# Performance work log

Measured on AMD Instinct MI355X. Metric: run time of the kernel, lower is better.

Reference implementation:

```python
import jax, jax.numpy as jnp
import numpy as np

EMBED = 1024
HEADS = 16
HEAD_DIM = EMBED // HEADS
NUM_BUCKETS = 32
MAX_DISTANCE = 128
B, L = 4, 2048


def relative_position_bucket(relative_position, num_buckets=NUM_BUCKETS, max_distance=MAX_DISTANCE):
    # Faithful port of the torch helper (unidirectional T5 bucketing).
    n = -relative_position                       # [L, L] int32
    max_exact = num_buckets // 2
    is_small = n < max_exact
    nf = jnp.maximum(n, 1).astype(jnp.float32)   # guard log(<=0); masked out by is_small
    val_if_large = max_exact + (
        jnp.log(nf / max_exact) / np.log(max_distance / max_exact) * (num_buckets - max_exact)
    ).astype(jnp.int32)                          # .long() in torch truncates; values >=0 here
    val_if_large = jnp.minimum(val_if_large, num_buckets - 1)
    ret = jnp.where(is_small, n, val_if_large)
    return jnp.maximum(ret, 0)


def setup_inputs() -> dict:
    key = jax.random.key(0)
    ks = jax.random.split(key, 11)
    s = 0.02
    return {
        "x": jax.random.normal(ks[0], (B, L, EMBED), dtype=jnp.float32),
        "wq": jax.random.normal(ks[1], (EMBED, EMBED), dtype=jnp.float32) * s,
        "bq": jnp.zeros((EMBED,), dtype=jnp.float32),
        "wk": jax.random.normal(ks[2], (EMBED, EMBED), dtype=jnp.float32) * s,
        "bk": jnp.zeros((EMBED,), dtype=jnp.float32),
        "wv": jax.random.normal(ks[3], (EMBED, EMBED), dtype=jnp.float32) * s,
        "bv": jnp.zeros((EMBED,), dtype=jnp.float32),
        "wo": jax.random.normal(ks[4], (EMBED, EMBED), dtype=jnp.float32) * s,
        "bo": jnp.zeros((EMBED,), dtype=jnp.float32),
        "rel_bias": jax.random.normal(ks[5], (NUM_BUCKETS, HEADS), dtype=jnp.float32) * s,
    }


def reference(x, wq, bq, wk, bk, wv, bv, wo, bo, rel_bias):
    Bx, Lx, C = x.shape
    # torch nn.Linear: y = x @ W.T + b
    def proj(w, b):
        y = jnp.einsum("blc,dc->bld", x, w) + b
        return y.reshape(Bx, Lx, HEADS, HEAD_DIM).transpose(0, 2, 1, 3)  # [B,H,L,Dh]
    q = proj(wq, bq)
    k = proj(wk, bk)
    v = proj(wv, bv)
    scores = jnp.einsum("bhqd,bhkd->bhqk", q, k) / np.sqrt(HEAD_DIM)  # [B,H,L,L]
    ctx = jnp.arange(Lx, dtype=jnp.int32)
    relative = ctx[None, :] - ctx[:, None]                            # [L,L]
    bucket_ids = relative_position_bucket(relative)                   # [L,L]
    bias = rel_bias[bucket_ids]                                       # [L,L,H]
    bias = jnp.transpose(bias, (2, 0, 1))                             # [H,L,L]
    attn = jax.nn.softmax(scores + bias[None], axis=-1)
    out = jnp.einsum("bhqk,bhkd->bhqd", attn, v)                      # [B,H,L,Dh]
    out = out.transpose(0, 2, 1, 3).reshape(Bx, Lx, C)
    return jnp.einsum("blc,dc->bld", out, wo) + bo
```

## Files before the change

kernel.cpp:

```cpp
#include <hip/hip_runtime.h>

typedef __bf16 bf16x8 __attribute__((ext_vector_type(8)));
typedef __bf16 bf16x2 __attribute__((ext_vector_type(2)));
typedef float f32x4 __attribute__((ext_vector_type(4)));
typedef float f32x16 __attribute__((ext_vector_type(16)));
typedef short short8v __attribute__((ext_vector_type(8)));
typedef unsigned uint4v __attribute__((ext_vector_type(4)));
typedef unsigned short ushort_t;

#define EMB 1024
#define HEADS 16
#define HDIM 64
#define BATCH 4
#define SEQ 2048
#define LOG2E 1.44269504088896340736f
#define FIXED_M 12.0f

__device__ __forceinline__ ushort_t f2bf(float f) {
  union { float f; unsigned u; } x; x.f = f;
  unsigned r = x.u + 0x7fffu + ((x.u >> 16) & 1u);
  return (ushort_t)(r >> 16);
}

__device__ __forceinline__ unsigned pack2(float lo, float hi) {
  bf16x2 t;
  t.x = (__bf16)lo;
  t.y = (__bf16)hi;
  return __builtin_bit_cast(unsigned, t);
}

__device__ __forceinline__ void gload_lds16(const void* g, void* l) {
  __builtin_amdgcn_global_load_lds(
      (const __attribute__((address_space(1))) void*)g,
      (__attribute__((address_space(3))) void*)l, 16, 0, 0);
}

__global__ __launch_bounds__(256) void convert_all(
    const float* __restrict__ x,
    const float* __restrict__ wq, const float* __restrict__ wk,
    const float* __restrict__ wv, const float* __restrict__ wo,
    ushort_t* __restrict__ xb, ushort_t* __restrict__ wqb,
    ushort_t* __restrict__ wkb, ushort_t* __restrict__ wvb,
    ushort_t* __restrict__ wob) {
  int cid = blockIdx.x * 256 + threadIdx.x;
  const float* src;
  ushort_t* dst;
  int off;
  if (cid < 1048576) {
    src = x; dst = xb; off = cid;
  } else {
    int r = cid - 1048576;
    int wi = r >> 17;
    off = r & 131071;
    src = wi == 0 ? wq : wi == 1 ? wk : wi == 2 ? wv : wo;
    dst = wi == 0 ? wqb : wi == 1 ? wkb : wi == 2 ? wvb : wob;
  }
  const float4* s4 = (const float4*)(src + (size_t)off * 8);
  float4 a = s4[0], b = s4[1];
  ushort_t tmp[8] = {f2bf(a.x), f2bf(a.y), f2bf(a.z), f2bf(a.w),
                     f2bf(b.x), f2bf(b.y), f2bf(b.z), f2bf(b.w)};
  *(short8v*)(dst + (size_t)off * 8) = *(const short8v*)tmp;
}

__global__ __launch_bounds__(256) void build_biasR(
    const float* __restrict__ rel_bias, float* __restrict__ biasR) {
  int fid = blockIdx.x * 256 + threadIdx.x;
  int hh = fid >> 12;
  int p = (fid >> 10) & 3;
  int j = fid & 1023;
#pragma unroll
  for (int e = 0; e < 4; ++e) {
    int r = 4 * j + p + e;
    int n = 2048 - r;
    int bucket;
    if (n < 16) {
      bucket = n > 0 ? n : 0;
    } else {
      float tt = logf((float)n * 0.0625f) * (16.0f / logf(8.0f));
      int v = 16 + (int)tt;
      bucket = v < 31 ? v : 31;
    }
    biasR[(size_t)fid * 4 + e] = rel_bias[bucket * HEADS + hh] * LOG2E - FIXED_M;
  }
}

__global__ __launch_bounds__(256) void gemm_qkv(
    const ushort_t* __restrict__ xb,
    const ushort_t* __restrict__ wqb, const ushort_t* __restrict__ wkb,
    const ushort_t* __restrict__ wvb,
    const float* __restrict__ bq, const float* __restrict__ bk,
    const float* __restrict__ bv,
    ushort_t* __restrict__ qb, ushort_t* __restrict__ kb,
    ushort_t* __restrict__ vtb) {
  const int wgid = blockIdx.x;
  const int xcd = wgid & 7;
  const int r0 = wgid >> 3;
  const int nb = r0 % 24;
  const int mb = (r0 / 24) * 8 + xcd;
  const int wsel = nb >> 3;
  const int nloc = (nb & 7) * 128;
  const ushort_t* W = wsel == 0 ? wqb : wsel == 1 ? wkb : wvb;
  const float* bias = wsel == 0 ? bq : wsel == 1 ? bk : bv;
  const float scale = wsel == 0 ? 0.125f * LOG2E : 1.0f;

  __shared__ ushort_t Al[128 * 64];
  __shared__ ushort_t Bl[128 * 64];
  const int tid = threadIdx.x, lane = tid & 63, wid = tid >> 6;
  const int wm = wid >> 1, wn = wid & 1;
  const int srow = lane >> 3;
  const int scol = (lane & 7) * 8;
  f32x4 acc[4][4] = {};

  for (int kt = 0; kt < EMB / 64; ++kt) {
    const int k0 = kt * 64;
#pragma unroll
    for (int i = 0; i < 4; ++i) {
      int c = i * 4 + wid;
      int row = c * 8 + srow;
      gload_lds16(xb + (size_t)(mb * 128 + row) * EMB + k0 + scol, &Al[c * 512]);
      gload_lds16(W + (size_t)(nloc + row) * EMB + k0 + scol, &Bl[c * 512]);
    }
    __syncthreads();
#pragma unroll
    for (int kk = 0; kk < 2; ++kk) {
      const int koff = kk * 32 + (lane >> 4) * 8;
      bf16x8 af[4], bfv[4];
#pragma unroll
      for (int m = 0; m < 4; ++m)
        af[m] = *(const bf16x8*)&Al[(wm * 64 + m * 16 + (lane & 15)) * 64 + koff];
#pragma unroll
      for (int n = 0; n < 4; ++n)
        bfv[n] = *(const bf16x8*)&Bl[(wn * 64 + n * 16 + (lane & 15)) * 64 + koff];
#pragma unroll
      for (int m = 0; m < 4; ++m)
#pragma unroll
        for (int n = 0; n < 4; ++n)
          acc[m][n] = __builtin_amdgcn_mfma_f32_16x16x32_bf16(af[m], bfv[n],
                                                              acc[m][n], 0, 0, 0);
    }
    __syncthreads();
  }

#pragma unroll
  for (int m = 0; m < 4; ++m)
#pragma unroll
    for (int n = 0; n < 4; ++n)
#pragma unroll
      for (int r = 0; r < 4; ++r) {
        int row = mb * 128 + wm * 64 + m * 16 + (lane >> 4) * 4 + r;
        int col = nloc + wn * 64 + n * 16 + (lane & 15);
        float v = (acc[m][n][r] + bias[col]) * scale;
        int b = row >> 11, l = row & 2047;
        int hh = col >> 6, d = col & 63;
        if (wsel == 2) {
          int lp = (l & ~12) | ((l & 4) << 1) | ((l & 8) >> 1);
          vtb[(((size_t)(b * HEADS + hh) * HDIM) + d) * SEQ + lp] = f2bf(v);
        } else {
          ushort_t* outp = wsel == 0 ? qb : kb;
          outp[(((size_t)(b * HEADS + hh) * SEQ) + l) * HDIM + d] = f2bf(v);
        }
      }
}

__global__ __launch_bounds__(256) void gemm_out(
    const ushort_t* __restrict__ ctxb, const ushort_t* __restrict__ wob,
    const float* __restrict__ bo, float* __restrict__ out) {
  const int wgid = blockIdx.x;
  const int xcd = wgid & 7;
  const int r0 = wgid >> 3;
  const int nb = r0 & 7;
  const int mb = (r0 >> 3) * 8 + xcd;
  __shared__ ushort_t Al[128 * 64];
  __shared__ ushort_t Bl[128 * 64];
  const int tid = threadIdx.x, lane = tid & 63, wid = tid >> 6;
  const int wm = wid >> 1, wn = wid & 1;
  const int srow = lane >> 3;
  const int scol = (lane & 7) * 8;
  f32x4 acc[4][4] = {};

  for (int kt = 0; kt < EMB / 64; ++kt) {
    const int k0 = kt * 64;
#pragma unroll
    for (int i = 0; i < 4; ++i) {
      int c = i * 4 + wid;
      int row = c * 8 + srow;
      gload_lds16(ctxb + (size_t)(mb * 128 + row) * EMB + k0 + scol, &Al[c * 512]);
      gload_lds16(wob + (size_t)(nb * 128 + row) * EMB + k0 + scol, &Bl[c * 512]);
    }
    __syncthreads();
#pragma unroll
    for (int kk = 0; kk < 2; ++kk) {
      const int koff = kk * 32 + (lane >> 4) * 8;
      bf16x8 af[4], bfv[4];
#pragma unroll
      for (int m = 0; m < 4; ++m)
        af[m] = *(const bf16x8*)&Al[(wm * 64 + m * 16 + (lane & 15)) * 64 + koff];
#pragma unroll
      for (int n = 0; n < 4; ++n)
        bfv[n] = *(const bf16x8*)&Bl[(wn * 64 + n * 16 + (lane & 15)) * 64 + koff];
#pragma unroll
      for (int m = 0; m < 4; ++m)
#pragma unroll
        for (int n = 0; n < 4; ++n)
          acc[m][n] = __builtin_amdgcn_mfma_f32_16x16x32_bf16(af[m], bfv[n],
                                                              acc[m][n], 0, 0, 0);
    }
    __syncthreads();
  }

#pragma unroll
  for (int m = 0; m < 4; ++m)
#pragma unroll
    for (int n = 0; n < 4; ++n)
#pragma unroll
      for (int r = 0; r < 4; ++r) {
        int row = mb * 128 + wm * 64 + m * 16 + (lane >> 4) * 4 + r;
        int col = nb * 128 + wn * 64 + n * 16 + (lane & 15);
        out[(size_t)row * EMB + col] = acc[m][n][r] + bo[col];
      }
}

__global__ __launch_bounds__(256) void attn(
    const ushort_t* __restrict__ qb, const ushort_t* __restrict__ kb,
    const ushort_t* __restrict__ vtb, const float* __restrict__ biasR,
    ushort_t* __restrict__ ctxb) {
  const int wgid = blockIdx.x;
  const int xcd = wgid & 7;
  const int sidx = wgid >> 3;
  const int qblk = sidx & 15;
  const int bh = ((sidx >> 4) << 3) | xcd;
  const int h = bh & 15, b = bh >> 4;
  const int tid = threadIdx.x;
  const int lane = tid & 63, w = tid >> 6;
  const int l31 = lane & 31, hi5 = lane >> 5;
  const int pidx = (lane ^ 32) << 2;

  __shared__ ushort_t SM[16384];

  const size_t base = (size_t)bh * (SEQ * HDIM);
  const int q = qblk * 128 + w * 32 + l31;

  bf16x8 qf[4];
#pragma unroll
  for (int s = 0; s < 4; ++s)
    qf[s] = *(const bf16x8*)&qb[base + (size_t)q * HDIM + s * 16 + hi5 * 8];

  int koA[4];
#pragma unroll
  for (int s = 0; s < 4; ++s)
    koA[s] = (s * 16 + hi5 * 8) ^ ((l31 & 7) << 3);
  const int rb0 = l31 * 64;
  const int rb1 = rb0 + 2048;

  const int p = (4 - (q & 3)) & 3;
  const int j00 = ((4 * hi5 - q + 2048) - p) >> 2;
  const float4* bptr = (const float4*)biasR + ((h * 4 + p) * 1024 + j00);

  const int chR0 = tid >> 3, chC0 = (tid & 7) * 8;
  const int chR1 = chR0 + 32;
  const int kd0 = chR0 * 64 + (chC0 ^ ((chR0 & 7) << 3));
  const int kd1 = chR1 * 64 + (chC0 ^ ((chR1 & 7) << 3));

  const ushort_t* kp0 = kb + base + (size_t)chR0 * HDIM + chC0;
  const ushort_t* kp1 = kb + base + (size_t)chR1 * HDIM + chC0;
  const ushort_t* vp0 = vtb + base + (size_t)chR0 * SEQ + chC0;
  const ushort_t* vp1 = vtb + base + (size_t)chR1 * SEQ + chC0;

  short8v kr0 = *(const short8v*)kp0;
  short8v kr1 = *(const short8v*)kp1;
  short8v vr0 = *(const short8v*)vp0;
  short8v vr1 = *(const short8v*)vp1;
  *(short8v*)&SM[kd0] = kr0;
  *(short8v*)&SM[kd1] = kr1;
  *(short8v*)&SM[4096 + kd0] = vr0;
  *(short8v*)&SM[4096 + kd1] = vr1;
  kp0 += 64 * HDIM; kp1 += 64 * HDIM; vp0 += 64; vp1 += 64;
  kr0 = *(const short8v*)kp0;
  kr1 = *(const short8v*)kp1;
  vr0 = *(const short8v*)vp0;
  vr1 = *(const short8v*)vp1;
  __syncthreads();

  f32x16 o0 = {}, o1 = {}, lv = {};

#pragma unroll 2
  for (int t = 0; t < 32; ++t) {
    const int c = t & 1;
    ushort_t* Kl = SM + c * 8192;
    ushort_t* Vl = Kl + 4096;

    float4 bw[8];
#pragma unroll
    for (int hh = 0; hh < 2; ++hh)
#pragma unroll
      for (int g = 0; g < 4; ++g)
        bw[hh * 4 + g] = bptr[hh * 8 + g * 2];

    f32x16 s0, s1;
#pragma unroll
    for (int r = 0; r < 16; ++r) {
      s0[r] = bw[r >> 2][r & 3];
      s1[r] = bw[4 + (r >> 2)][r & 3];
    }
    __builtin_amdgcn_s_setprio(1);
#pragma unroll
    for (int s = 0; s < 4; ++s) {
      bf16x8 ka = *(const bf16x8*)&Kl[rb0 + koA[s]];
      s0 = __builtin_amdgcn_mfma_f32_32x32x16_bf16(ka, qf[s], s0, 0, 0, 0);
    }
#pragma unroll
    for (int s = 0; s < 4; ++s) {
      bf16x8 ka = *(const bf16x8*)&Kl[rb1 + koA[s]];
      s1 = __builtin_amdgcn_mfma_f32_32x32x16_bf16(ka, qf[s], s1, 0, 0, 0);
    }
    __builtin_amdgcn_s_setprio(0);

    if (t < 31) {
      ushort_t* Kn = SM + (c ^ 1) * 8192;
      *(short8v*)&Kn[kd0] = kr0;
      *(short8v*)&Kn[kd1] = kr1;
      *(short8v*)&Kn[4096 + kd0] = vr0;
      *(short8v*)&Kn[4096 + kd1] = vr1;
      kp0 += 64 * HDIM; kp1 += 64 * HDIM; vp0 += 64; vp1 += 64;
      kr0 = *(const short8v*)kp0;
      kr1 = *(const short8v*)kp1;
      vr0 = *(const short8v*)vp0;
      vr1 = *(const short8v*)vp1;
    }

#pragma unroll
    for (int r = 0; r < 16; ++r) s0[r] = __builtin_amdgcn_exp2f(s0[r]);
#pragma unroll
    for (int r = 0; r < 16; ++r) s1[r] = __builtin_amdgcn_exp2f(s1[r]);
    lv += s0;
    lv += s1;

    unsigned pk0[8], pk1[8];
#pragma unroll
    for (int d = 0; d < 8; ++d) {
      pk0[d] = pack2(s0[2 * d], s0[2 * d + 1]);
      pk1[d] = pack2(s1[2 * d], s1[2 * d + 1]);
    }
    bf16x8 paf[4];
    {
      uint4v t0 = {pk0[0], pk0[1], pk0[2], pk0[3]};
      uint4v t1 = {pk0[4], pk0[5], pk0[6], pk0[7]};
      uint4v t2 = {pk1[0], pk1[1], pk1[2], pk1[3]};
      uint4v t3 = {pk1[4], pk1[5], pk1[6], pk1[7]};
      paf[0] = __builtin_bit_cast(bf16x8, t0);
      paf[1] = __builtin_bit_cast(bf16x8, t1);
      paf[2] = __builtin_bit_cast(bf16x8, t2);
      paf[3] = __builtin_bit_cast(bf16x8, t3);
    }

    __builtin_amdgcn_s_setprio(1);
#pragma unroll
    for (int ss = 0; ss < 4; ++ss) {
      bf16x8 vb0 = *(const bf16x8*)&Vl[rb0 + koA[ss]];
      bf16x8 vb1 = *(const bf16x8*)&Vl[rb1 + koA[ss]];
      o0 = __builtin_amdgcn_mfma_f32_32x32x16_bf16(paf[ss], vb0, o0, 0, 0, 0);
      o1 = __builtin_amdgcn_mfma_f32_32x32x16_bf16(paf[ss], vb1, o1, 0, 0, 0);
    }
    __builtin_amdgcn_s_setprio(0);

    if (t < 31) __syncthreads();
    bptr += 16;
  }

  float li = (((lv[0] + lv[1]) + (lv[2] + lv[3])) +
              ((lv[4] + lv[5]) + (lv[6] + lv[7]))) +
             (((lv[8] + lv[9]) + (lv[10] + lv[11])) +
              ((lv[12] + lv[13]) + (lv[14] + lv[15])));
  float li2 = __int_as_float(
      __builtin_amdgcn_ds_bpermute(pidx, __float_as_int(li)));
  li += li2;
  float inv = 1.0f / li;
#pragma unroll
  for (int r = 0; r < 16; ++r) {
    int qr = (r & 3) + 8 * (r >> 2) + 4 * hi5;
    float iv = __int_as_float(
        __builtin_amdgcn_ds_bpermute(qr << 2, __float_as_int(inv)));
    o0[r] *= iv;
    o1[r] *= iv;
  }
  ushort_t* T = SM + w * 2048;
#pragma unroll
  for (int r = 0; r < 16; ++r) {
    int qr = (r & 3) + 8 * (r >> 2) + 4 * hi5;
    int sw = (qr & 7) << 3;
    T[qr * 64 + (l31 ^ sw)] = f2bf(o0[r]);
    T[qr * 64 + ((32 + l31) ^ sw)] = f2bf(o1[r]);
  }
  const int qr2 = lane >> 1;
  const int dh0 = (lane & 1) * 32;
  const int sw2 = (qr2 & 7) << 3;
  const size_t crow =
      ((size_t)b * SEQ + qblk * 128 + w * 32 + qr2) * EMB + h * 64;
#pragma unroll
  for (int c = 0; c < 4; ++c) {
    short8v vv = *(const short8v*)&T[qr2 * 64 + ((dh0 + c * 8) ^ sw2)];
    *(short8v*)&ctxb[crow + dh0 + c * 8] = vv;
  }
}

extern "C" void kernel_launch(void* const* d_in, const int* in_sizes, int n_in,
                              void* d_out, int out_size, void* d_ws, size_t ws_size,
                              hipStream_t stream) {
  const float* x = (const float*)d_in[0];
  const float* wq = (const float*)d_in[1];
  const float* bq = (const float*)d_in[2];
  const float* wk = (const float*)d_in[3];
  const float* bk = (const float*)d_in[4];
  const float* wv = (const float*)d_in[5];
  const float* bv = (const float*)d_in[6];
  const float* wo = (const float*)d_in[7];
  const float* bo = (const float*)d_in[8];
  const float* rel_bias = (const float*)d_in[9];
  float* out = (float*)d_out;

  char* ws = (char*)d_ws;
  ushort_t* xb  = (ushort_t*)(ws);
  ushort_t* wqb = (ushort_t*)(ws + 16777216);
  ushort_t* wkb = (ushort_t*)(ws + 16777216 + 2097152);
  ushort_t* wvb = (ushort_t*)(ws + 16777216 + 2 * 2097152);
  ushort_t* wob = (ushort_t*)(ws + 16777216 + 3 * 2097152);
  ushort_t* qb  = (ushort_t*)(ws + 25165824);
  ushort_t* kb  = (ushort_t*)(ws + 25165824 + 16777216);
  ushort_t* vtb = (ushort_t*)(ws + 25165824 + 2 * 16777216);
  float* biasR  = (float*)(ws + 75497472);
  ushort_t* ctxb = xb;

  convert_all<<<6144, 256, 0, stream>>>(x, wq, wk, wv, wo, xb, wqb, wkb, wvb, wob);
  build_biasR<<<256, 256, 0, stream>>>(rel_bias, biasR);
  gemm_qkv<<<1536, 256, 0, stream>>>(xb, wqb, wkb, wvb, bq, bk, bv, qb, kb, vtb);
  attn<<<1024, 256, 0, stream>>>(qb, kb, vtb, biasR, ctxb);
  gemm_out<<<512, 256, 0, stream>>>(ctxb, wob, bo, out);
}
```

Baseline: 272.5 us.

## Stream K/V tiles into LDS with direct global-to-LDS loads

Replaces the register-staged K/V prefetch (global load into VGPRs, then ds_write into the other buffer) with a gload_lds16 helper that copies global memory straight into the double-buffered LDS tiles. The swizzle moves from the LDS write address to the global column offset. This frees the staging registers and drops the explicit LDS store instructions. It also shrinks the row-sum accumulator from 16 to 4 floats to cut register pressure. Correctness now depends on the async LDS loads completing before the barrier and on the new swizzle matching the read pattern.

```diff
diff --git a/kernel.cpp b/kernel.cpp
--- a/kernel.cpp
+++ b/kernel.cpp
@@ -256,38 +256,30 @@
   const int j00 = ((4 * hi5 - q + 2048) - p) >> 2;
   const float4* bptr = (const float4*)biasR + ((h * 4 + p) * 1024 + j00);
 
-  const int chR0 = tid >> 3, chC0 = (tid & 7) * 8;
-  const int chR1 = chR0 + 32;
-  const int kd0 = chR0 * 64 + (chC0 ^ ((chR0 & 7) << 3));
-  const int kd1 = chR1 * 64 + (chC0 ^ ((chR1 & 7) << 3));
-
-  const ushort_t* kp0 = kb + base + (size_t)chR0 * HDIM + chC0;
-  const ushort_t* kp1 = kb + base + (size_t)chR1 * HDIM + chC0;
-  const ushort_t* vp0 = vtb + base + (size_t)chR0 * SEQ + chC0;
-  const ushort_t* vp1 = vtb + base + (size_t)chR1 * SEQ + chC0;
-
-  short8v kr0 = *(const short8v*)kp0;
-  short8v kr1 = *(const short8v*)kp1;
-  short8v vr0 = *(const short8v*)vp0;
-  short8v vr1 = *(const short8v*)vp1;
-  *(short8v*)&SM[kd0] = kr0;
-  *(short8v*)&SM[kd1] = kr1;
-  *(short8v*)&SM[4096 + kd0] = vr0;
-  *(short8v*)&SM[4096 + kd1] = vr1;
+  const int srowK = lane >> 3;
+  const int scol8 = ((lane & 7) ^ srowK) * 8;
+  const int row0 = w * 16 + srowK;
+  const ushort_t* kp0 = kb + base + (size_t)row0 * HDIM + scol8;
+  const ushort_t* kp1 = kp0 + 8 * HDIM;
+  const ushort_t* vp0 = vtb + base + (size_t)row0 * SEQ + scol8;
+  const ushort_t* vp1 = vp0 + 8 * SEQ;
+  const int kdst0 = (2 * w) * 512, kdst1 = kdst0 + 512;
+
+  gload_lds16(kp0, SM + kdst0);
+  gload_lds16(kp1, SM + kdst1);
+  gload_lds16(vp0, SM + 4096 + kdst0);
+  gload_lds16(vp1, SM + 4096 + kdst1);
   kp0 += 64 * HDIM; kp1 += 64 * HDIM; vp0 += 64; vp1 += 64;
-  kr0 = *(const short8v*)kp0;
-  kr1 = *(const short8v*)kp1;
-  vr0 = *(const short8v*)vp0;
-  vr1 = *(const short8v*)vp1;
   __syncthreads();
 
-  f32x16 o0 = {}, o1 = {}, lv = {};
+  f32x16 o0 = {}, o1 = {};
+  f32x4 lv4 = {};
 
 #pragma unroll 2
   for (int t = 0; t < 32; ++t) {
-    const int c = t & 1;
-    ushort_t* Kl = SM + c * 8192;
-    ushort_t* Vl = Kl + 4096;
+    const int cbuf = (t & 1) * 8192;
+    const ushort_t* Kl = SM + cbuf;
+    const ushort_t* Vl = Kl + 4096;
 
     float4 bw[8];
 #pragma unroll
@@ -316,24 +308,22 @@
     __builtin_amdgcn_s_setprio(0);
 
     if (t < 31) {
-      ushort_t* Kn = SM + (c ^ 1) * 8192;
-      *(short8v*)&Kn[kd0] = kr0;
-      *(short8v*)&Kn[kd1] = kr1;
-      *(short8v*)&Kn[4096 + kd0] = vr0;
-      *(short8v*)&Kn[4096 + kd1] = vr1;
+      const int nbuf = ((t + 1) & 1) * 8192;
+      gload_lds16(kp0, SM + nbuf + kdst0);
+      gload_lds16(kp1, SM + nbuf + kdst1);
+      gload_lds16(vp0, SM + nbuf + 4096 + kdst0);
+      gload_lds16(vp1, SM + nbuf + 4096 + kdst1);
       kp0 += 64 * HDIM; kp1 += 64 * HDIM; vp0 += 64; vp1 += 64;
-      kr0 = *(const short8v*)kp0;
-      kr1 = *(const short8v*)kp1;
-      vr0 = *(const short8v*)vp0;
-      vr1 = *(const short8v*)vp1;
     }
 
 #pragma unroll
     for (int r = 0; r < 16; ++r) s0[r] = __builtin_amdgcn_exp2f(s0[r]);
 #pragma unroll
     for (int r = 0; r < 16; ++r) s1[r] = __builtin_amdgcn_exp2f(s1[r]);
-    lv += s0;
-    lv += s1;
+#pragma unroll
+    for (int r = 0; r < 4; ++r)
+      lv4[r] += ((s0[r] + s0[4 + r]) + (s0[8 + r] + s0[12 + r])) +
+                ((s1[r] + s1[4 + r]) + (s1[8 + r] + s1[12 + r]));
 
     unsigned pk0[8], pk1[8];
 #pragma unroll
@@ -367,10 +357,7 @@
     bptr += 16;
   }
 
-  float li = (((lv[0] + lv[1]) + (lv[2] + lv[3])) +
-              ((lv[4] + lv[5]) + (lv[6] + lv[7]))) +
-             (((lv[8] + lv[9]) + (lv[10] + lv[11])) +
-              ((lv[12] + lv[13]) + (lv[14] + lv[15])));
+  float li = (lv4[0] + lv4[1]) + (lv4[2] + lv4[3]);
   float li2 = __int_as_float(
       __builtin_amdgcn_ds_bpermute(pidx, __float_as_int(li)));
   li += li2;
```

New measurement: 274.3 us. About the same (+0.6%).
